# Performance work log

Hardware: AMD Instinct MI355X
Metric: run time of the kernel (lower is better)

## Reference

```python
import jax, jax.numpy as jnp
import numpy as np

N_HEAD = 16
D_K = 64
D_V = 64
EMBED = 1024
BATCH = 4
SEQ = 2048

def setup_inputs() -> dict:
    key = jax.random.key(0)
    ks = jax.random.split(key, 12)
    s = lambda d: 1.0 / np.sqrt(d)
    u = lambda k, shape, d: jax.random.uniform(k, shape, jnp.float32, -s(d), s(d))
    return {
        'z': jax.random.normal(ks[0], (BATCH, SEQ, EMBED), jnp.float32),
        'wq': u(ks[1], (EMBED, D_K), D_K),
        'wk': u(ks[2], (EMBED, D_K), D_K),
        'wv': u(ks[3], (EMBED, D_V), D_V),
        'fcq_w': u(ks[4], (D_K, N_HEAD * D_K), D_K),
        'fcq_b': u(ks[5], (N_HEAD * D_K,), N_HEAD * D_K),
        'fck_w': u(ks[6], (D_K, N_HEAD * D_K), D_K),
        'fck_b': u(ks[7], (N_HEAD * D_K,), N_HEAD * D_K),
        'fcv_w': u(ks[8], (D_V, N_HEAD * D_V), D_V),
        'fcv_b': u(ks[9], (N_HEAD * D_V,), N_HEAD * D_V),
        'fco_w': u(ks[10], (N_HEAD * D_V, EMBED), EMBED),
        'fco_b': u(ks[11], (EMBED,), EMBED),
    }

def reference(z, wq, wk, wv, fcq_w, fcq_b, fck_w, fck_b, fcv_w, fcv_b, fco_w, fco_b):
    b, n, _ = z.shape
    scale = jnp.sqrt(jnp.float32(D_K))
    # bottleneck projections then per-head expansion
    q = (z @ wq) @ fcq_w + fcq_b  # [b, n, H*dk]
    k = (z @ wk) @ fck_w + fck_b  # [b, n, H*dk]
    v = (z @ wv) @ fcv_w + fcv_b  # [b, n, H*dv]
    q = q.reshape(b, n, N_HEAD, D_K)
    k = k.reshape(b, n, N_HEAD, D_K)
    v = v.reshape(b, n, N_HEAD, D_V)
    scores = jnp.einsum('bihd,bjhd->bhij', q, k) / scale  # [b, H, n, n]
    attn = jax.nn.softmax(scores, axis=-1)
    out = jnp.einsum('bhij,bjhd->bihd', attn, v)  # [b, n, H, dv]
    out = out.reshape(b, n, N_HEAD * D_V)
    return out @ fco_w + fco_b  # [b, n, embed]
```

## Files before the change

### kernel.cpp

```cpp
#include <hip/hip_runtime.h>


typedef __bf16 bf16x8 __attribute__((ext_vector_type(8)));
typedef __bf16 bf16x4 __attribute__((ext_vector_type(4)));
typedef __bf16 bf16x2 __attribute__((ext_vector_type(2)));
typedef float floatx4 __attribute__((ext_vector_type(4)));
typedef float floatx16 __attribute__((ext_vector_type(16)));
typedef unsigned int uintx4 __attribute__((ext_vector_type(4)));
typedef unsigned int uintx2 __attribute__((ext_vector_type(2)));

#define LDP 72

#define SW64(row, col) (((row) << 6) | (((((col) >> 3) ^ ((row) & 7) ^ (((row) >> 3) & 7)) << 3) | ((col) & 7)))

#if __has_builtin(__builtin_amdgcn_exp2f)
__device__ __forceinline__ float fast_exp2(float x) { return __builtin_amdgcn_exp2f(x); }
#else
__device__ __forceinline__ float fast_exp2(float x) { return exp2f(x); }
#endif

__device__ __forceinline__ unsigned int pack_bf16(float lo, float hi) {
    bf16x2 w; w[0] = (__bf16)lo; w[1] = (__bf16)hi;
    return __builtin_bit_cast(unsigned int, w);
}
__device__ __forceinline__ unsigned int pack2(__bf16 lo, __bf16 hi) {
    bf16x2 w; w[0] = lo; w[1] = hi;
    return __builtin_bit_cast(unsigned int, w);
}
#if __has_builtin(__builtin_amdgcn_permlane32_swap)
__device__ __forceinline__ void xchg(unsigned int& X, unsigned int& Y, int) {
    uintx2 r = __builtin_amdgcn_permlane32_swap(X, Y, false, false);
    X = r[0]; Y = r[1];
}
#else
__device__ __forceinline__ void xchg(unsigned int& X, unsigned int& Y, int hl) {
    unsigned int sX = (unsigned int)__shfl_xor((int)X, 32);
    unsigned int sY = (unsigned int)__shfl_xor((int)Y, 32);
    unsigned int lo = hl ? sY : X;
    unsigned int hi = hl ? Y : sX;
    X = lo; Y = hi;
}
#endif
__device__ __forceinline__ bf16x8 frag4(unsigned int a, unsigned int b, unsigned int c, unsigned int d) {
    uintx4 u; u[0] = a; u[1] = b; u[2] = c; u[3] = d;
    return __builtin_bit_cast(bf16x8, u);
}

__global__ void detect_dtype(const unsigned short* __restrict__ z, int* __restrict__ flag) {
    __shared__ int cnt;
    if (threadIdx.x == 0) cnt = 0;
    __syncthreads();
    int local = 0;
    for (int i = threadIdx.x; i < 16384; i += 256) {
        unsigned int u = (unsigned int)z[i] << 16;
        float x = __uint_as_float(u);
        float ax = fabsf(x);
        if (!(ax <= 1024.0f) || (x != 0.0f && ax < 1e-20f)) local++;
    }
    atomicAdd(&cnt, local);
    __syncthreads();
    if (threadIdx.x == 0) *flag = (cnt > 1310) ? 1 : 0;
}

struct ConvArgs { const void* src[12]; int n[12]; int off[12]; };

__global__ void convert_inputs(ConvArgs a, __bf16* __restrict__ cv, const int* __restrict__ flag,
                               int base_k) {
    const int k = blockIdx.y + base_k;
    const int i = (blockIdx.x * 256 + threadIdx.x) * 8;
    if (i >= a.n[k]) return;
    __bf16* dst = cv + a.off[k] + i;
    if (*flag) {
        const float* s = (const float*)a.src[k] + i;
        float4 f0 = *(const float4*)s;
        float4 f1 = *(const float4*)(s + 4);
        bf16x8 v;
        v[0] = (__bf16)f0.x; v[1] = (__bf16)f0.y; v[2] = (__bf16)f0.z; v[3] = (__bf16)f0.w;
        v[4] = (__bf16)f1.x; v[5] = (__bf16)f1.y; v[6] = (__bf16)f1.z; v[7] = (__bf16)f1.w;
        *(bf16x8*)dst = v;
    } else {
        *(bf16x8*)dst = *(const bf16x8*)((const __bf16*)a.src[k] + i);
    }
}

__global__ __launch_bounds__(256) void gemm_bias(
    const __bf16* __restrict__ A0, const __bf16* __restrict__ A1, const __bf16* __restrict__ A2,
    const __bf16* __restrict__ B0, const __bf16* __restrict__ B1, const __bf16* __restrict__ B2,
    const __bf16* __restrict__ bias0, const __bf16* __restrict__ bias1, const __bf16* __restrict__ bias2,
    void* __restrict__ C0, void* __restrict__ C1, void* __restrict__ C2,
    int M, int N, int K, int has_bias, const int* flagp,
    float os0, float os1, float os2)
{
    const int zsel = blockIdx.z;
    const __bf16* A = (zsel == 0) ? A0 : (zsel == 1) ? A1 : A2;
    const __bf16* B = (zsel == 0) ? B0 : (zsel == 1) ? B1 : B2;
    const __bf16* bias = (zsel == 0) ? bias0 : (zsel == 1) ? bias1 : bias2;
    void* C = (zsel == 0) ? C0 : (zsel == 1) ? C1 : C2;
    const float oscale = (zsel == 0) ? os0 : (zsel == 1) ? os1 : os2;
    const int out_fp32 = flagp ? *flagp : 0;

    const int m0 = blockIdx.x * 128;
    const int n0 = blockIdx.y * 64;
    const int tid = threadIdx.x;
    const int wave = tid >> 6;
    const int ln = tid & 15;
    const int quad = (tid >> 4) & 3;

    __shared__ __bf16 As[128 * LDP];
    __shared__ __bf16 Bts[64 * 64];

    floatx4 acc[2][4] = {};

    for (int k0 = 0; k0 < K; k0 += 64) {
        __syncthreads();
        for (int i = tid; i < 1024; i += 256) {
            int r = i >> 3, c8 = (i & 7) << 3;
            *(bf16x8*)&As[r * LDP + c8] = *(const bf16x8*)&A[(m0 + r) * K + k0 + c8];
        }
        for (int i = tid; i < 512; i += 256) {
            int kk = i >> 3, a8 = (i & 7) << 3;
            bf16x8 v = *(const bf16x8*)&B[(k0 + kk) * N + n0 + a8];
            #pragma unroll
            for (int j = 0; j < 8; j++) Bts[SW64(a8 + j, kk)] = v[j];
        }
        __syncthreads();
        #pragma unroll
        for (int ks = 0; ks < 2; ks++) {
            bf16x8 a[2], b[4];
            a[0] = *(const bf16x8*)&As[(wave * 32 + ln) * LDP + ks * 32 + quad * 8];
            a[1] = *(const bf16x8*)&As[(wave * 32 + 16 + ln) * LDP + ks * 32 + quad * 8];
            #pragma unroll
            for (int nt = 0; nt < 4; nt++)
                b[nt] = *(const bf16x8*)&Bts[SW64(nt * 16 + ln, ks * 32 + quad * 8)];
            #pragma unroll
            for (int rt = 0; rt < 2; rt++)
                #pragma unroll
                for (int nt = 0; nt < 4; nt++)
                    acc[rt][nt] = __builtin_amdgcn_mfma_f32_16x16x32_bf16(a[rt], b[nt], acc[rt][nt], 0, 0, 0);
        }
    }
    #pragma unroll
    for (int rt = 0; rt < 2; rt++) {
        const int row = m0 + wave * 32 + rt * 16 + quad * 4;
        #pragma unroll
        for (int nt = 0; nt < 4; nt++) {
            const int col = n0 + nt * 16 + ln;
            float bv = has_bias ? (float)bias[col] : 0.0f;
            #pragma unroll
            for (int r = 0; r < 4; r++) {
                float val = (acc[rt][nt][r] + bv) * oscale;
                if (out_fp32) ((float*)C)[(row + r) * N + col] = val;
                else ((__bf16*)C)[(row + r) * N + col] = (__bf16)val;
            }
        }
    }
}

__global__ __launch_bounds__(256, 3) void attn_kernel(
    const __bf16* __restrict__ Qg, const __bf16* __restrict__ Kg,
    const __bf16* __restrict__ Vg, __bf16* __restrict__ Og)
{
    const int bh = blockIdx.x;
    const int b = bh >> 4, h = bh & 15;
    const int q0 = blockIdx.y * 128;
    const int base = b * 2048 * 1024 + h * 64;
    const int tid = threadIdx.x;
    const int wave = tid >> 6, ln = tid & 63;
    const int l31 = ln & 31, hl = ln >> 5;
    const int h8 = hl * 8;

    __shared__ __bf16 Ks[2][64 * 64];
    __shared__ __bf16 VTs[2][64 * 64];

    bf16x8 qf[4];
    #pragma unroll
    for (int ks = 0; ks < 4; ks++)
        qf[ks] = *(const bf16x8*)&Qg[base + (q0 + wave * 32 + l31) * 1024 + ks * 16 + h8];

    const int kr = tid >> 3, kc = (tid & 7) << 3;
    const int vr2 = (tid >> 3) * 2, vc = (tid & 7) << 3;

    {
        bf16x8 ka = *(const bf16x8*)&Kg[base + kr * 1024 + kc];
        bf16x8 kb = *(const bf16x8*)&Kg[base + (kr + 32) * 1024 + kc];
        bf16x8 va = *(const bf16x8*)&Vg[base + vr2 * 1024 + vc];
        bf16x8 vb = *(const bf16x8*)&Vg[base + (vr2 + 1) * 1024 + vc];
        *(bf16x8*)&Ks[0][SW64(kr, kc)] = ka;
        *(bf16x8*)&Ks[0][SW64(kr + 32, kc)] = kb;
        #pragma unroll
        for (int j = 0; j < 8; j++)
            *(unsigned int*)&VTs[0][SW64(vc + j, vr2)] = pack2(va[j], vb[j]);
    }

    floatx16 o_acc[2] = {};
    float m_i = -1e30f, l_i = 0.0f;

    for (int t = 0; t < 32; t++) {
        const int cur = t & 1, nxt = cur ^ 1;
        bf16x8 nka, nkb, nva, nvb;
        if (t < 31) {
            const int kvn = (t + 1) * 64;
            nka = *(const bf16x8*)&Kg[base + (kvn + kr) * 1024 + kc];
            nkb = *(const bf16x8*)&Kg[base + (kvn + kr + 32) * 1024 + kc];
            nva = *(const bf16x8*)&Vg[base + (kvn + vr2) * 1024 + vc];
            nvb = *(const bf16x8*)&Vg[base + (kvn + vr2 + 1) * 1024 + vc];
        }
        __syncthreads();

        floatx16 sv[2] = {};
        #pragma unroll
        for (int ks = 0; ks < 4; ks++) {
            bf16x8 a0 = *(const bf16x8*)&Ks[cur][SW64(l31, ks * 16 + h8)];
            bf16x8 a1 = *(const bf16x8*)&Ks[cur][SW64(32 + l31, ks * 16 + h8)];
            sv[0] = __builtin_amdgcn_mfma_f32_32x32x16_bf16(a0, qf[ks], sv[0], 0, 0, 0);
            sv[1] = __builtin_amdgcn_mfma_f32_32x32x16_bf16(a1, qf[ks], sv[1], 0, 0, 0);
        }

        float m8[8];
        #pragma unroll
        for (int r = 0; r < 8; r++)
            m8[r] = fmaxf(fmaxf(sv[0][r], sv[0][r + 8]), fmaxf(sv[1][r], sv[1][r + 8]));
        float mx = fmaxf(fmaxf(fmaxf(m8[0], m8[4]), fmaxf(m8[1], m8[5])),
                         fmaxf(fmaxf(m8[2], m8[6]), fmaxf(m8[3], m8[7])));
        mx = fmaxf(mx, __shfl_xor(mx, 32));

        if (__any(mx > m_i + 8.0f)) {
            float m_new = fmaxf(m_i, mx);
            float alpha = fast_exp2(m_i - m_new);
            m_i = m_new;
            l_i *= alpha;
            #pragma unroll
            for (int dt = 0; dt < 2; dt++)
                #pragma unroll
                for (int r = 0; r < 16; r++) o_acc[dt][r] *= alpha;
        }

        float p0[16], p1[16];
        #pragma unroll
        for (int r = 0; r < 16; r++) p0[r] = fast_exp2(sv[0][r] - m_i);
        #pragma unroll
        for (int r = 0; r < 16; r++) p1[r] = fast_exp2(sv[1][r] - m_i);
        float rsA = 0.f, rsB = 0.f, rsC = 0.f, rsD = 0.f;
        #pragma unroll
        for (int r = 0; r < 16; r += 4) {
            rsA += p0[r]; rsB += p0[r + 1]; rsC += p0[r + 2]; rsD += p0[r + 3];
            rsA += p1[r]; rsB += p1[r + 1]; rsC += p1[r + 2]; rsD += p1[r + 3];
        }
        float rs = (rsA + rsB) + (rsC + rsD);
        rs += __shfl_xor(rs, 32);
        l_i += rs;

        bf16x8 pf0, pf1, pf2, pf3;
        {
            unsigned int A0 = pack_bf16(p0[0], p0[1]),  B0 = pack_bf16(p0[2], p0[3]);
            unsigned int C0 = pack_bf16(p0[4], p0[5]),  D0 = pack_bf16(p0[6], p0[7]);
            unsigned int A1 = pack_bf16(p0[8], p0[9]),  B1 = pack_bf16(p0[10], p0[11]);
            unsigned int C1 = pack_bf16(p0[12], p0[13]), D1 = pack_bf16(p0[14], p0[15]);
            xchg(A0, C0, hl); xchg(B0, D0, hl); xchg(A1, C1, hl); xchg(B1, D1, hl);
            pf0 = frag4(A0, B0, C0, D0);
            pf1 = frag4(A1, B1, C1, D1);
        }
        {
            unsigned int A0 = pack_bf16(p1[0], p1[1]),  B0 = pack_bf16(p1[2], p1[3]);
            unsigned int C0 = pack_bf16(p1[4], p1[5]),  D0 = pack_bf16(p1[6], p1[7]);
            unsigned int A1 = pack_bf16(p1[8], p1[9]),  B1 = pack_bf16(p1[10], p1[11]);
            unsigned int C1 = pack_bf16(p1[12], p1[13]), D1 = pack_bf16(p1[14], p1[15]);
            xchg(A0, C0, hl); xchg(B0, D0, hl); xchg(A1, C1, hl); xchg(B1, D1, hl);
            pf2 = frag4(A0, B0, C0, D0);
            pf3 = frag4(A1, B1, C1, D1);
        }

        if (t < 31) {
            *(bf16x8*)&Ks[nxt][SW64(kr, kc)] = nka;
            *(bf16x8*)&Ks[nxt][SW64(kr + 32, kc)] = nkb;
        }

        #pragma unroll
        for (int js = 0; js < 4; js++) {
            bf16x8 av0 = *(const bf16x8*)&VTs[cur][SW64(l31, js * 16 + h8)];
            bf16x8 av1 = *(const bf16x8*)&VTs[cur][SW64(32 + l31, js * 16 + h8)];
            bf16x8 pb = (js == 0) ? pf0 : (js == 1) ? pf1 : (js == 2) ? pf2 : pf3;
            o_acc[0] = __builtin_amdgcn_mfma_f32_32x32x16_bf16(av0, pb, o_acc[0], 0, 0, 0);
            o_acc[1] = __builtin_amdgcn_mfma_f32_32x32x16_bf16(av1, pb, o_acc[1], 0, 0, 0);
        }

        if (t < 31) {
            #pragma unroll
            for (int j = 0; j < 8; j++)
                *(unsigned int*)&VTs[nxt][SW64(vc + j, vr2)] = pack2(nva[j], nvb[j]);
        }
    }

    float inv = 1.0f / l_i;
    const int orow = q0 + wave * 32 + l31;
    #pragma unroll
    for (int dt = 0; dt < 2; dt++)
        #pragma unroll
        for (int g = 0; g < 4; g++) {
            bf16x4 ov;
            #pragma unroll
            for (int e = 0; e < 4; e++) ov[e] = (__bf16)(o_acc[dt][g * 4 + e] * inv);
            *(bf16x4*)&Og[base + orow * 1024 + dt * 32 + g * 8 + hl * 4] = ov;
        }
}

extern "C" void kernel_launch(void* const* d_in, const int* in_sizes, int n_in,
                              void* d_out, int out_size, void* d_ws, size_t ws_size,
                              hipStream_t stream)
{
    int* flag = (int*)d_ws;
    __bf16* cv = (__bf16*)((char*)d_ws + 256);

    const int Z = 0, WQ = 8388608, WK = 8454144, WV = 8519680;
    const int FCQW = 8585216, FCKW = 8650752, FCVW = 8716288, FCOW = 8781824;
    const int FCQB = 9830400, FCKB = 9831424, FCVB = 9832448, FCOB = 9833472;
    __bf16* zb = cv + 10485760;
    __bf16* Qw = cv + 12582912;
    __bf16* Kw = Qw + 8388608;
    __bf16* Vw = Kw + 8388608;
    __bf16* Ow = cv + Z;

    detect_dtype<<<1, 256, 0, stream>>>((const unsigned short*)d_in[0], flag);

    ConvArgs ca;
    const int offs[12] = {Z, WQ, WK, WV, FCQW, FCQB, FCKW, FCKB, FCVW, FCVB, FCOW, FCOB};
    for (int i = 0; i < 12; i++) { ca.src[i] = d_in[i]; ca.n[i] = in_sizes[i]; ca.off[i] = offs[i]; }
    convert_inputs<<<dim3(4096, 1), 256, 0, stream>>>(ca, cv, flag, 0);
    convert_inputs<<<dim3(512, 11), 256, 0, stream>>>(ca, cv, flag, 1);

    gemm_bias<<<dim3(64, 1, 3), 256, 0, stream>>>(
        cv + Z, cv + Z, cv + Z, cv + WQ, cv + WK, cv + WV,
        cv + FCQB, cv + FCQB, cv + FCQB,
        zb, zb + 524288, zb + 1048576, 8192, 64, 1024, 0, nullptr,
        1.0f, 1.0f, 1.0f);

    const float QSC = 0.125f * 1.44269504088896f;
    gemm_bias<<<dim3(64, 16, 3), 256, 0, stream>>>(
        zb, zb + 524288, zb + 1048576,
        cv + FCQW, cv + FCKW, cv + FCVW, cv + FCQB, cv + FCKB, cv + FCVB,
        Qw, Kw, Vw, 8192, 1024, 64, 1, nullptr,
        QSC, 1.0f, 1.0f);

    attn_kernel<<<dim3(64, 16), 256, 0, stream>>>(Qw, Kw, Vw, Ow);

    gemm_bias<<<dim3(64, 16, 1), 256, 0, stream>>>(
        Ow, Ow, Ow, cv + FCOW, cv + FCOW, cv + FCOW, cv + FCOB, cv + FCOB, cv + FCOB,
        d_out, d_out, d_out, 8192, 1024, 1024, 1, flag,
        1.0f, 1.0f, 1.0f);
}
```

Baseline: 318.7 us.

## Add 128x128 async-LDS GEMM with pre-transposed weights for expansion and output projections

```diff
diff --git a/kernel.cpp b/kernel.cpp
--- a/kernel.cpp
+++ b/kernel.cpp
@@ -44,6 +44,11 @@
 __device__ __forceinline__ bf16x8 frag4(unsigned int a, unsigned int b, unsigned int c, unsigned int d) {
     uintx4 u; u[0] = a; u[1] = b; u[2] = c; u[3] = d;
     return __builtin_bit_cast(bf16x8, u);
+}
+__device__ __forceinline__ void async_b128(const __bf16* g, __bf16* l) {
+    __builtin_amdgcn_global_load_lds(
+        (const __attribute__((address_space(1))) unsigned int*)g,
+        (__attribute__((address_space(3))) unsigned int*)l, 16, 0, 0);
 }
 
 __global__ void detect_dtype(const unsigned short* __restrict__ z, int* __restrict__ flag) {
@@ -83,6 +88,31 @@
     }
 }
 
+__global__ __launch_bounds__(256) void transpose_w(
+    const __bf16* __restrict__ in, __bf16* __restrict__ out, int K,
+    int zsin, int zsout)
+{
+    in  += blockIdx.z * zsin;
+    out += blockIdx.z * zsout;
+    __shared__ __bf16 t[64][72];
+    const int bn = blockIdx.x * 64, bk = blockIdx.y * 64;
+    const int r = threadIdx.x >> 3, c8 = (threadIdx.x & 7) << 3;
+    #pragma unroll
+    for (int p = 0; p < 2; p++) {
+        bf16x8 v = *(const bf16x8*)&in[(bk + p * 32 + r) * 1024 + bn + c8];
+        #pragma unroll
+        for (int j = 0; j < 8; j++) t[c8 + j][p * 32 + r] = v[j];
+    }
+    __syncthreads();
+    #pragma unroll
+    for (int p = 0; p < 2; p++) {
+        bf16x8 v;
+        #pragma unroll
+        for (int j = 0; j < 8; j++) v[j] = t[p * 32 + r][c8 + j];
+        *(bf16x8*)&out[(bn + p * 32 + r) * K + bk + c8] = v;
+    }
+}
+
 __global__ __launch_bounds__(256) void gemm_bias(
     const __bf16* __restrict__ A0, const __bf16* __restrict__ A1, const __bf16* __restrict__ A2,
     const __bf16* __restrict__ B0, const __bf16* __restrict__ B1, const __bf16* __restrict__ B2,
@@ -156,6 +186,80 @@
     }
 }
 
+__global__ __launch_bounds__(256, 2) void gemm128(
+    const __bf16* __restrict__ A0, const __bf16* __restrict__ A1, const __bf16* __restrict__ A2,
+    const __bf16* __restrict__ BT0, const __bf16* __restrict__ BT1, const __bf16* __restrict__ BT2,
+    const __bf16* __restrict__ bias0, const __bf16* __restrict__ bias1, const __bf16* __restrict__ bias2,
+    void* __restrict__ C0, void* __restrict__ C1, void* __restrict__ C2,
+    int M, int N, int K, const int* flagp,
+    float os0, float os1, float os2)
+{
+    const int zsel = blockIdx.z;
+    const __bf16* A = (zsel == 0) ? A0 : (zsel == 1) ? A1 : A2;
+    const __bf16* BT = (zsel == 0) ? BT0 : (zsel == 1) ? BT1 : BT2;
+    const __bf16* bias = (zsel == 0) ? bias0 : (zsel == 1) ? bias1 : bias2;
+    void* C = (zsel == 0) ? C0 : (zsel == 1) ? C1 : C2;
+    const float oscale = (zsel == 0) ? os0 : (zsel == 1) ? os1 : os2;
+    const int out_fp32 = flagp ? *flagp : 0;
+
+    const int m0 = blockIdx.x * 128;
+    const int n0 = blockIdx.y * 128;
+    const int tid = threadIdx.x;
+    const int wave = tid >> 6, ln = tid & 63;
+    const int wr = wave >> 1, wc = wave & 1;
+    const int l15 = tid & 15, quad = (tid >> 4) & 3;
+
+    __shared__ __bf16 As[128 * 64];
+    __shared__ __bf16 Bs[128 * 64];
+
+    const int r_off = ln >> 3, j_off = ln & 7;
+
+    floatx4 acc[4][4] = {};
+
+    for (int k0 = 0; k0 < K; k0 += 64) {
+        __syncthreads();
+        #pragma unroll
+        for (int it = 0; it < 4; it++) {
+            const int seg = wave * 4 + it;
+            const int row = seg * 8 + r_off;
+            const int c = j_off ^ (row & 7) ^ ((row >> 3) & 7);
+            async_b128(&A[(m0 + row) * K + k0 + c * 8], &As[seg * 512]);
+            async_b128(&BT[(n0 + row) * K + k0 + c * 8], &Bs[seg * 512]);
+        }
+        __syncthreads();
+        #pragma unroll
+        for (int ks = 0; ks < 2; ks++) {
+            bf16x8 a[4], b[4];
+            #pragma unroll
+            for (int rt = 0; rt < 4; rt++)
+                a[rt] = *(const bf16x8*)&As[SW64(wr * 64 + rt * 16 + l15, ks * 32 + quad * 8)];
+            #pragma unroll
+            for (int nt = 0; nt < 4; nt++)
+                b[nt] = *(const bf16x8*)&Bs[SW64(wc * 64 + nt * 16 + l15, ks * 32 + quad * 8)];
+            #pragma unroll
+            for (int rt = 0; rt < 4; rt++)
+                #pragma unroll
+                for (int nt = 0; nt < 4; nt++)
+                    acc[rt][nt] = __builtin_amdgcn_mfma_f32_16x16x32_bf16(a[rt], b[nt], acc[rt][nt], 0, 0, 0);
+        }
+    }
+    #pragma unroll
+    for (int rt = 0; rt < 4; rt++) {
+        const int row = m0 + wr * 64 + rt * 16 + quad * 4;
+        #pragma unroll
+        for (int nt = 0; nt < 4; nt++) {
+            const int col = n0 + wc * 64 + nt * 16 + l15;
+            float bv = (float)bias[col];
+            #pragma unroll
+            for (int r = 0; r < 4; r++) {
+                float val = (acc[rt][nt][r] + bv) * oscale;
+                if (out_fp32) ((float*)C)[(row + r) * N + col] = val;
+                else ((__bf16*)C)[(row + r) * N + col] = (__bf16)val;
+            }
+        }
+    }
+}
+
 __global__ __launch_bounds__(256, 3) void attn_kernel(
     const __bf16* __restrict__ Qg, const __bf16* __restrict__ Kg,
     const __bf16* __restrict__ Vg, __bf16* __restrict__ Og)
@@ -319,6 +423,8 @@
     __bf16* Kw = Qw + 8388608;
     __bf16* Vw = Kw + 8388608;
     __bf16* Ow = cv + Z;
+    __bf16* WT3 = cv + WQ;
+    __bf16* OWT = zb;
 
     detect_dtype<<<1, 256, 0, stream>>>((const unsigned short*)d_in[0], flag);
 
@@ -334,17 +440,23 @@
         zb, zb + 524288, zb + 1048576, 8192, 64, 1024, 0, nullptr,
         1.0f, 1.0f, 1.0f);
 
+    transpose_w<<<dim3(16, 1, 3), 256, 0, stream>>>(cv + FCQW, WT3, 64, 65536, 65536);
+
     const float QSC = 0.125f * 1.44269504088896f;
-    gemm_bias<<<dim3(64, 16, 3), 256, 0, stream>>>(
+    gemm128<<<dim3(64, 8, 3), 256, 0, stream>>>(
         zb, zb + 524288, zb + 1048576,
-        cv + FCQW, cv + FCKW, cv + FCVW, cv + FCQB, cv + FCKB, cv + FCVB,
-        Qw, Kw, Vw, 8192, 1024, 64, 1, nullptr,
+        WT3, WT3 + 65536, WT3 + 131072,
+        cv + FCQB, cv + FCKB, cv + FCVB,
+        Qw, Kw, Vw, 8192, 1024, 64, nullptr,
         QSC, 1.0f, 1.0f);
 
+    transpose_w<<<dim3(16, 16, 1), 256, 0, stream>>>(cv + FCOW, OWT, 1024, 0, 0);
+
     attn_kernel<<<dim3(64, 16), 256, 0, stream>>>(Qw, Kw, Vw, Ow);
 
-    gemm_bias<<<dim3(64, 16, 1), 256, 0, stream>>>(
-        Ow, Ow, Ow, cv + FCOW, cv + FCOW, cv + FCOW, cv + FCOB, cv + FCOB, cv + FCOB,
-        d_out, d_out, d_out, 8192, 1024, 1024, 1, flag,
+    gemm128<<<dim3(64, 8, 1), 256, 0, stream>>>(
+        Ow, Ow, Ow, OWT, OWT, OWT,
+        cv + FCOB, cv + FCOB, cv + FCOB,
+        d_out, d_out, d_out, 8192, 1024, 1024, flag,
         1.0f, 1.0f, 1.0f);
 }
```

Result: no change. 314.0 us (-1.5%).
